# Kernel optimization log

Measured on AMD Instinct MI355X. Metric: run time of the kernel, lower is better.

## Reference

```python
import jax, jax.numpy as jnp
import numpy as np

HIDDEN = 1024
INTER = 4096

def setup_inputs() -> dict:
    key = jax.random.key(0)
    k1, k2, k3, k4, k5 = jax.random.split(key, 5)
    hidden_states = jax.random.normal(k1, (4, 2048, HIDDEN), dtype=jnp.float32)
    # Linear params: W stored pre-transposed as [in, out], matching W = dense.weight.t()
    W1 = jax.random.normal(k2, (HIDDEN, INTER), dtype=jnp.float32) * (1.0 / np.sqrt(HIDDEN))
    b1 = jax.random.normal(k3, (INTER,), dtype=jnp.float32) * 0.02
    W2 = jax.random.normal(k4, (INTER, HIDDEN), dtype=jnp.float32) * (1.0 / np.sqrt(INTER))
    b2 = jax.random.normal(k5, (HIDDEN,), dtype=jnp.float32) * 0.02
    return {"hidden_states": hidden_states, "W1": W1, "b1": b1, "W2": W2, "b2": b2}

def reference(hidden_states, W1, b1, W2, b2):
    # Tiled loops in the original are exactly a dense 2-layer MLP with ReLU.
    h = jax.nn.relu(jnp.einsum('bsh,hi->bsi', hidden_states, W1) + b1)
    return jnp.einsum('bsi,ih->bsh', h, W2) + b2
```

## Files before the change

kernel.cpp:

```cpp
#include <hip/hip_runtime.h>
#include <cstddef>

typedef short short8 __attribute__((ext_vector_type(8)));
typedef unsigned short ushort8 __attribute__((ext_vector_type(8)));
typedef float f32x4 __attribute__((ext_vector_type(4)));

#define AS1(p) ((const __attribute__((address_space(1))) void*)(p))
#define AS3(p) ((__attribute__((address_space(3))) void*)(p))

__device__ __forceinline__ unsigned short f2bf(float f) {
  unsigned int u = __builtin_bit_cast(unsigned int, f);
  u += 0x7FFFu + ((u >> 16) & 1u);
  return (unsigned short)(u >> 16);
}

__device__ __forceinline__ void gload_lds16(const void* g, void* l) {
  __builtin_amdgcn_global_load_lds(AS1(g), AS3(l), 16, 0, 0);
}

__global__ void cvt_f32_bf16(const float* __restrict__ in,
                             unsigned short* __restrict__ out, int n4) {
  int i = blockIdx.x * blockDim.x + threadIdx.x;
  if (i >= n4) return;
  float4 v = *reinterpret_cast<const float4*>(in + (size_t)i * 4);
  ushort4 o;
  o.x = f2bf(v.x); o.y = f2bf(v.y); o.z = f2bf(v.z); o.w = f2bf(v.w);
  *reinterpret_cast<ushort4*>(out + (size_t)i * 4) = o;
}

__global__ void transpose_cvt(const float* __restrict__ in,
                              unsigned short* __restrict__ out,
                              int Kd, int Nd) {
  __shared__ float tile[32][33];
  const int n0 = blockIdx.x * 32;
  const int k0 = blockIdx.y * 32;
  const int tx = threadIdx.x;
  const int ty = threadIdx.y;
#pragma unroll
  for (int i = 0; i < 4; ++i)
    tile[ty + i * 8][tx] = in[(size_t)(k0 + ty + i * 8) * Nd + n0 + tx];
  __syncthreads();
#pragma unroll
  for (int i = 0; i < 4; ++i)
    out[(size_t)(n0 + ty + i * 8) * Kd + k0 + tx] = f2bf(tile[tx][ty + i * 8]);
}

#define PH(ABUF, BBUF, H, KK, STAGE, WAITC)                                    \
  {                                                                            \
    if ((H) == 0) {                                                            \
      _Pragma("unroll")                                                        \
      for (int ni = 0; ni < NB; ++ni)                                          \
        bfr[ni] = *reinterpret_cast<const short8*>((BBUF) + bread[ni][KK]);    \
    }                                                                          \
    short8 afr[4];                                                             \
    _Pragma("unroll")                                                          \
    for (int m2 = 0; m2 < 4; ++m2)                                             \
      afr[m2] = *reinterpret_cast<const short8*>((ABUF) + aread[(H)*4+m2][KK]);\
    STAGE;                                                                     \
    __builtin_amdgcn_s_barrier();                                              \
    asm volatile("s_waitcnt lgkmcnt(0)" ::: "memory");                         \
    __builtin_amdgcn_sched_barrier(0);                                         \
    __builtin_amdgcn_s_setprio(1);                                             \
    _Pragma("unroll")                                                          \
    for (int m2 = 0; m2 < 4; ++m2) {                                           \
      _Pragma("unroll")                                                        \
      for (int ni = 0; ni < NB; ++ni)                                          \
        acc[(H)*4+m2][ni] = __builtin_amdgcn_mfma_f32_16x16x32_bf16(           \
            afr[m2], bfr[ni], acc[(H)*4+m2][ni], 0, 0, 0);                     \
    }                                                                          \
    __builtin_amdgcn_s_setprio(0);                                             \
    WAITC;                                                                     \
    __builtin_amdgcn_s_barrier();                                              \
  }

template <int BN, int RELU_BF16_OUT>
__global__ __launch_bounds__(512, 2)
void gemm8p(const unsigned short* __restrict__ A, int lda,
            const unsigned short* __restrict__ Bp, int ldb,
            const float* __restrict__ bias,
            void* __restrict__ C, int ldc, int K, int nbx) {
  constexpr int PWN     = BN / 4;
  constexpr int NB      = PWN / 16;
  constexpr int LOADS_B = BN / 128;
  constexpr int BHROWS  = BN / 2;
  constexpr int BHSZ    = BHROWS * 128;
  extern __shared__ char lds[];
  char* const A0b = lds;
  char* const A1b = lds + 32768;
  char* const B0b = lds + 65536;
  char* const B1b = lds + 65536 + 2 * BHSZ;

  const int tid  = threadIdx.x;
  const int lane = tid & 63;
  const int wid  = tid >> 6;
  const int wm   = wid >> 2;
  const int wn   = wid & 3;

  const int cpx     = gridDim.x >> 3;
  const int logical = (blockIdx.x & 7) * cpx + (blockIdx.x >> 3);
  const int bx = logical % nbx;
  const int by = logical / nbx;
  const int m0 = by * 256;
  const int n0 = bx * BN;

  f32x4 acc[8][NB];
#pragma unroll
  for (int i = 0; i < 8; ++i)
#pragma unroll
    for (int j = 0; j < NB; ++j)
      acc[i][j] = (f32x4){0.f, 0.f, 0.f, 0.f};

  size_t aofs0, aofs1, bofs0, bofs1 = 0;
  {
    int sr = tid * 16, nat = sr ^ (((sr >> 7) & 7) << 4);
    aofs0 = (size_t)(m0 + (nat >> 7)) * lda + ((nat & 127) >> 1);
    bofs0 = (size_t)(n0 + (nat >> 7)) * ldb + ((nat & 127) >> 1);
    sr = (512 + tid) * 16; nat = sr ^ (((sr >> 7) & 7) << 4);
    aofs1 = (size_t)(m0 + (nat >> 7)) * lda + ((nat & 127) >> 1);
    if (LOADS_B == 2)
      bofs1 = (size_t)(n0 + (nat >> 7)) * ldb + ((nat & 127) >> 1);
  }
  const int dst0 = (tid & 448) * 16;
  const int dst1 = dst0 + 8192;

  auto stA = [&](char* ab, int half, int kel) {
    gload_lds16(A + aofs0 + (size_t)half * 128 * lda + kel, ab + half * 16384 + dst0);
    gload_lds16(A + aofs1 + (size_t)half * 128 * lda + kel, ab + half * 16384 + dst1);
  };
  auto stB = [&](char* bb, int half, int kel) {
    gload_lds16(Bp + bofs0 + (size_t)half * BHROWS * ldb + kel, bb + half * BHSZ + dst0);
    if constexpr (LOADS_B == 2)
      gload_lds16(Bp + bofs1 + (size_t)half * BHROWS * ldb + kel, bb + half * BHSZ + dst1);
  };
  auto waitLB = [&]() {
    if constexpr (LOADS_B == 2) asm volatile("s_waitcnt vmcnt(2)" ::: "memory");
    else                        asm volatile("s_waitcnt vmcnt(1)" ::: "memory");
  };

  int aread[8][2], bread[NB][2];
#pragma unroll
  for (int mi = 0; mi < 8; ++mi)
#pragma unroll
    for (int kk = 0; kk < 2; ++kk) {
      int nat = (wm * 128 + mi * 16 + (lane & 15)) * 128 + kk * 64 + (lane >> 4) * 16;
      aread[mi][kk] = nat ^ (((nat >> 7) & 7) << 4);
    }
#pragma unroll
  for (int ni = 0; ni < NB; ++ni)
#pragma unroll
    for (int kk = 0; kk < 2; ++kk) {
      int nat = (wn * PWN + ni * 16 + (lane & 15)) * 128 + kk * 64 + (lane >> 4) * 16;
      bread[ni][kk] = nat ^ (((nat >> 7) & 7) << 4);
    }

  stB(B0b, 0, 0);
  stB(B0b, 1, 0);
  stA(A0b, 0, 0);
  stA(A0b, 1, 0);
  stB(B1b, 0, 64);
  waitLB();
  __builtin_amdgcn_s_barrier();

  const int niter = K >> 7;
  for (int it = 0; it < niter; ++it) {
    const bool last = (it == niter - 1);
    const int kb = it << 7;
    short8 bfr[NB];
    PH(A0b, B0b, 0, 0, stB(B1b, 1, kb + 64), ((void)0));
    PH(A0b, B0b, 1, 0, stA(A1b, 0, kb + 64), ((void)0));
    PH(A0b, B0b, 0, 1, stA(A1b, 1, kb + 64), ((void)0));
    PH(A0b, B0b, 1, 1, { if (!last) stB(B0b, 0, kb + 128); },
       { if (last) { asm volatile("s_waitcnt vmcnt(0)" ::: "memory"); } else waitLB(); });
    PH(A1b, B1b, 0, 0, { if (!last) stB(B0b, 1, kb + 128); }, ((void)0));
    PH(A1b, B1b, 1, 0, { if (!last) stA(A0b, 0, kb + 128); }, ((void)0));
    PH(A1b, B1b, 0, 1, { if (!last) stA(A0b, 1, kb + 128); }, ((void)0));
    PH(A1b, B1b, 1, 1, { if (!last) stB(B1b, 0, kb + 192); },
       { if (!last) waitLB(); });
  }

  const int row0 = m0 + wm * 128 + (lane >> 4) * 4;
  const int col0 = n0 + wn * PWN + (lane & 15);
#pragma unroll
  for (int ni = 0; ni < NB; ++ni) {
    const int c = col0 + ni * 16;
    const float bv = bias[c];
#pragma unroll
    for (int mi = 0; mi < 8; ++mi) {
#pragma unroll
      for (int r = 0; r < 4; ++r) {
        const size_t idx = (size_t)(row0 + mi * 16 + r) * ldc + c;
        float v = acc[mi][ni][r] + bv;
        if (RELU_BF16_OUT) {
          v = v > 0.f ? v : 0.f;
          ((unsigned short*)C)[idx] = f2bf(v);
        } else {
          ((float*)C)[idx] = v;
        }
      }
    }
  }
}

template <int A_F32, int RELU_BF16_OUT>
__global__ __launch_bounds__(256, 2)
void gemm_bf16(const void* __restrict__ Ap, int lda,
               const unsigned short* __restrict__ B, int ldb,
               const float* __restrict__ bias,
               void* __restrict__ C, int ldc,
               int K, int beta) {
  __shared__ char lds[32768];
  char* const As = lds;
  char* const Bs = lds + 16384;

  const int tid  = threadIdx.x;
  const int lane = tid & 63;
  const int w    = tid >> 6;
  const int wm   = w >> 1;
  const int wn   = w & 1;
  const int m0   = blockIdx.y * 128;
  const int n0   = blockIdx.x * 128;

  f32x4 acc[4][4];
#pragma unroll
  for (int i = 0; i < 4; ++i)
#pragma unroll
    for (int j = 0; j < 4; ++j)
      acc[i][j] = (f32x4){0.f, 0.f, 0.f, 0.f};

  int srow[4], scol[4], sbase[4];
#pragma unroll
  for (int j = 0; j < 4; ++j) {
    const int stored  = (j * 256 + tid) * 16;
    const int natural = stored ^ (((stored >> 7) & 7) << 4);
    srow[j]  = natural >> 7;
    scol[j]  = (natural & 127) >> 1;
    sbase[j] = (j * 256 + (tid & 192)) * 16;
  }

  size_t agofs[4];
  int ast[4];
  if (A_F32) {
#pragma unroll
    for (int p = 0; p < 4; ++p) {
      const int idx = p * 256 + tid;
      const int r   = idx >> 3;
      const int kbe = (idx & 7) * 8;
      agofs[p] = (size_t)(m0 + r) * lda + kbe;
      const int nat = r * 128 + kbe * 2;
      ast[p] = nat ^ (((nat >> 7) & 7) << 4);
    }
  }

  const int nsteps = K >> 6;
  for (int ks = 0; ks < nsteps; ++ks) {
    const int k0 = ks << 6;
    if (A_F32) {
      const float* Af = (const float*)Ap;
#pragma unroll
      for (int p = 0; p < 4; ++p) {
        const float* s = Af + agofs[p] + k0;
        float4 x0 = *reinterpret_cast<const float4*>(s);
        float4 x1 = *reinterpret_cast<const float4*>(s + 4);
        ushort8 v;
        v[0] = f2bf(x0.x); v[1] = f2bf(x0.y); v[2] = f2bf(x0.z); v[3] = f2bf(x0.w);
        v[4] = f2bf(x1.x); v[5] = f2bf(x1.y); v[6] = f2bf(x1.z); v[7] = f2bf(x1.w);
        *reinterpret_cast<ushort8*>(As + ast[p]) = v;
      }
    } else {
      const unsigned short* Ab = (const unsigned short*)Ap;
#pragma unroll
      for (int j = 0; j < 4; ++j)
        gload_lds16(Ab + (size_t)(m0 + srow[j]) * lda + (k0 + scol[j]),
                    As + sbase[j]);
    }
#pragma unroll
    for (int j = 0; j < 4; ++j)
      gload_lds16(B + (size_t)(n0 + srow[j]) * ldb + (k0 + scol[j]),
                  Bs + sbase[j]);
    __syncthreads();

#pragma unroll
    for (int kk = 0; kk < 2; ++kk) {
      const int kb = kk * 64 + (lane >> 4) * 16;
      short8 af[4], bfv[4];
#pragma unroll
      for (int mi = 0; mi < 4; ++mi) {
        int nat = (wm * 64 + mi * 16 + (lane & 15)) * 128 + kb;
        int st  = nat ^ (((nat >> 7) & 7) << 4);
        af[mi] = *reinterpret_cast<const short8*>(As + st);
      }
#pragma unroll
      for (int ni = 0; ni < 4; ++ni) {
        int nat = (wn * 64 + ni * 16 + (lane & 15)) * 128 + kb;
        int st  = nat ^ (((nat >> 7) & 7) << 4);
        bfv[ni] = *reinterpret_cast<const short8*>(Bs + st);
      }
#pragma unroll
      for (int mi = 0; mi < 4; ++mi)
#pragma unroll
        for (int ni = 0; ni < 4; ++ni)
          acc[mi][ni] = __builtin_amdgcn_mfma_f32_16x16x32_bf16(
              af[mi], bfv[ni], acc[mi][ni], 0, 0, 0);
    }
    __syncthreads();
  }

  const int row0 = m0 + wm * 64 + (lane >> 4) * 4;
  const int col0 = n0 + wn * 64 + (lane & 15);
#pragma unroll
  for (int ni = 0; ni < 4; ++ni) {
    const int c = col0 + ni * 16;
    const float bv = beta ? 0.f : bias[c];
#pragma unroll
    for (int mi = 0; mi < 4; ++mi) {
#pragma unroll
      for (int r = 0; r < 4; ++r) {
        const size_t idx = (size_t)(row0 + mi * 16 + r) * ldc + c;
        float v = acc[mi][ni][r] + bv;
        if (RELU_BF16_OUT) {
          v = v > 0.f ? v : 0.f;
          ((unsigned short*)C)[idx] = f2bf(v);
        } else {
          if (beta) v += ((float*)C)[idx];
          ((float*)C)[idx] = v;
        }
      }
    }
  }
}

extern "C" void kernel_launch(void* const* d_in, const int* in_sizes, int n_in,
                              void* d_out, int out_size, void* d_ws, size_t ws_size,
                              hipStream_t stream) {
  const float* X  = (const float*)d_in[0];
  const float* W1 = (const float*)d_in[1];
  const float* b1 = (const float*)d_in[2];
  const float* W2 = (const float*)d_in[3];
  const float* b2 = (const float*)d_in[4];
  float* out = (float*)d_out;

  const int M = 8192, H = 1024, I = 4096;
  const size_t MB = 1024 * 1024;

  char* ws = (char*)d_ws;
  unsigned short* W1t = (unsigned short*)ws;
  unsigned short* W2t = (unsigned short*)(ws + 8 * MB);

  transpose_cvt<<<dim3(I / 32, H / 32), dim3(32, 8), 0, stream>>>(W1, W1t, H, I);
  transpose_cvt<<<dim3(H / 32, I / 32), dim3(32, 8), 0, stream>>>(W2, W2t, I, H);

  if (ws_size >= 80 * MB) {
    unsigned short* Xbf = (unsigned short*)((char*)d_out + 16 * MB);
    unsigned short* Hbf = (unsigned short*)(ws + 16 * MB);
    int n4 = (M * H) / 4;
    cvt_f32_bf16<<<(n4 + 255) / 256, 256, 0, stream>>>(X, Xbf, n4);
    gemm8p<256, 1><<<512, 512, 131072, stream>>>(Xbf, H, W1t, H, b1, Hbf, I, H, I / 256);
    gemm8p<128, 0><<<256, 512, 98304, stream>>>(Hbf, I, W2t, I, b2, out, H, I, H / 128);
    return;
  }

  int Ic, useXbf;
  unsigned short* Xbf = nullptr;
  unsigned short* Hc;
  if (ws_size >= 64 * MB) {
    Ic = 2048; useXbf = 1;
    Xbf = (unsigned short*)(ws + 16 * MB);
    Hc  = (unsigned short*)(ws + 32 * MB);
  } else if (ws_size >= 48 * MB) {
    Ic = 1024; useXbf = 1;
    Xbf = (unsigned short*)(ws + 16 * MB);
    Hc  = (unsigned short*)(ws + 32 * MB);
  } else if (ws_size >= 32 * MB) {
    Ic = 1024; useXbf = 0;
    Hc  = (unsigned short*)(ws + 16 * MB);
  } else if (ws_size >= 24 * MB) {
    Ic = 512;  useXbf = 0;
    Hc  = (unsigned short*)(ws + 16 * MB);
  } else if (ws_size >= 20 * MB) {
    Ic = 256;  useXbf = 0;
    Hc  = (unsigned short*)(ws + 16 * MB);
  } else {
    Ic = 128;  useXbf = 0;
    Hc  = (unsigned short*)(ws + 16 * MB);
  }

  if (useXbf) {
    int n4 = (M * H) / 4;
    cvt_f32_bf16<<<(n4 + 255) / 256, 256, 0, stream>>>(X, Xbf, n4);
  }

  const int nch = I / Ic;
  for (int c = 0; c < nch; ++c) {
    const int i0 = c * Ic;
    if (useXbf)
      gemm_bf16<0, 1><<<dim3(Ic / 128, M / 128), 256, 0, stream>>>(
          Xbf, H, W1t + (size_t)i0 * H, H, b1 + i0, Hc, Ic, H, 0);
    else
      gemm_bf16<1, 1><<<dim3(Ic / 128, M / 128), 256, 0, stream>>>(
          X, H, W1t + (size_t)i0 * H, H, b1 + i0, Hc, Ic, H, 0);
    gemm_bf16<0, 0><<<dim3(H / 128, M / 128), 256, 0, stream>>>(
        Hc, Ic, W2t + i0, I, b2, out, H, Ic, c > 0);
  }
}
```

Baseline: 165.4 us.

## Restage GEMM LDS buffers by K-half for finer-grained prefetch pipeline

```diff
diff --git a/kernel.cpp b/kernel.cpp
--- a/kernel.cpp
+++ b/kernel.cpp
@@ -16,6 +16,11 @@
 
 __device__ __forceinline__ void gload_lds16(const void* g, void* l) {
   __builtin_amdgcn_global_load_lds(AS1(g), AS3(l), 16, 0, 0);
+}
+
+template <int N>
+__device__ __forceinline__ void vwait() {
+  asm volatile("s_waitcnt vmcnt(%0)" :: "n"(N) : "memory");
 }
 
 __global__ void cvt_f32_bf16(const float* __restrict__ in,
@@ -45,18 +50,21 @@
     out[(size_t)(n0 + ty + i * 8) * Kd + k0 + tx] = f2bf(tile[tx][ty + i * 8]);
 }
 
-#define PH(ABUF, BBUF, H, KK, STAGE, WAITC)                                    \
+#define PHASE(D, KK, MH, STAGE, WAIT)                                          \
   {                                                                            \
-    if ((H) == 0) {                                                            \
+    char* ab = lds + (D) * 32768 + (KK) * 16384;                               \
+    if ((MH) == 0) {                                                           \
+      char* bb = lds + 65536 + (D) * 2 * BKH + (KK) * BKH;                     \
       _Pragma("unroll")                                                        \
       for (int ni = 0; ni < NB; ++ni)                                          \
-        bfr[ni] = *reinterpret_cast<const short8*>((BBUF) + bread[ni][KK]);    \
+        bfr[ni] = *reinterpret_cast<const short8*>(bb + brd[ni]);              \
     }                                                                          \
     short8 afr[4];                                                             \
     _Pragma("unroll")                                                          \
     for (int m2 = 0; m2 < 4; ++m2)                                             \
-      afr[m2] = *reinterpret_cast<const short8*>((ABUF) + aread[(H)*4+m2][KK]);\
+      afr[m2] = *reinterpret_cast<const short8*>(ab + ard[(MH) * 4 + m2]);     \
     STAGE;                                                                     \
+    __builtin_amdgcn_sched_barrier(0);                                         \
     __builtin_amdgcn_s_barrier();                                              \
     asm volatile("s_waitcnt lgkmcnt(0)" ::: "memory");                         \
     __builtin_amdgcn_sched_barrier(0);                                         \
@@ -65,30 +73,27 @@
     for (int m2 = 0; m2 < 4; ++m2) {                                           \
       _Pragma("unroll")                                                        \
       for (int ni = 0; ni < NB; ++ni)                                          \
-        acc[(H)*4+m2][ni] = __builtin_amdgcn_mfma_f32_16x16x32_bf16(           \
-            afr[m2], bfr[ni], acc[(H)*4+m2][ni], 0, 0, 0);                     \
+        acc[(MH) * 4 + m2][ni] = __builtin_amdgcn_mfma_f32_16x16x32_bf16(      \
+            afr[m2], bfr[ni], acc[(MH) * 4 + m2][ni], 0, 0, 0);                \
     }                                                                          \
     __builtin_amdgcn_s_setprio(0);                                             \
-    WAITC;                                                                     \
+    WAIT;                                                                      \
     __builtin_amdgcn_s_barrier();                                              \
   }
 
 template <int BN, int RELU_BF16_OUT>
 __global__ __launch_bounds__(512, 2)
-void gemm8p(const unsigned short* __restrict__ A, int lda,
-            const unsigned short* __restrict__ Bp, int ldb,
-            const float* __restrict__ bias,
-            void* __restrict__ C, int ldc, int K, int nbx) {
+void gemm_kh(const unsigned short* __restrict__ A, int lda,
+             const unsigned short* __restrict__ B, int ldb,
+             const float* __restrict__ bias,
+             void* __restrict__ C, int ldc, int K, int nbx) {
+  constexpr int NB      = BN / 64;
   constexpr int PWN     = BN / 4;
-  constexpr int NB      = PWN / 16;
-  constexpr int LOADS_B = BN / 128;
-  constexpr int BHROWS  = BN / 2;
-  constexpr int BHSZ    = BHROWS * 128;
+  constexpr int BKH     = BN * 64;
+  constexpr int BL      = BN / 128;
+  constexpr int WSTEADY = 2 + 2 * BL;
+  constexpr int NSH     = (BN == 256) ? 7 : 6;
   extern __shared__ char lds[];
-  char* const A0b = lds;
-  char* const A1b = lds + 32768;
-  char* const B0b = lds + 65536;
-  char* const B1b = lds + 65536 + 2 * BHSZ;
 
   const int tid  = threadIdx.x;
   const int lane = tid & 63;
@@ -110,72 +115,83 @@
     for (int j = 0; j < NB; ++j)
       acc[i][j] = (f32x4){0.f, 0.f, 0.f, 0.f};
 
-  size_t aofs0, aofs1, bofs0, bofs1 = 0;
+  size_t aG[2];
+  size_t bG[2];
+#pragma unroll
+  for (int u = 0; u < 2; ++u) {
+    const int s    = (u * 512 + tid) * 16;
+    const int nat  = s ^ (((s >> 7) & 7) << 4);
+    const int line = nat >> 7;
+    const int boff = nat & 127;
+    const int sub  = (boff >> 6) & 1;
+    const int kel  = (boff & 63) >> 1;
+    aG[u] = (size_t)(m0 + sub * 128 + line) * lda + kel;
+    if (u < BL) {
+      const int brow = sub * (BN / 2) + line;
+      bG[u] = (size_t)(n0 + brow) * ldb + kel;
+    } else {
+      bG[u] = 0;
+    }
+  }
+  const int wbase = wid * 1024;
+
+  auto stage_a = [&](int d, int kk, int t) {
+    char* dst = lds + d * 32768 + kk * 16384;
+    const size_t kofs = (size_t)t * 64 + kk * 32;
+    gload_lds16(A + aG[0] + kofs, dst + wbase);
+    gload_lds16(A + aG[1] + kofs, dst + 8192 + wbase);
+  };
+  auto stage_b = [&](int d, int kk, int t) {
+    char* dst = lds + 65536 + d * 2 * BKH + kk * BKH;
+    const size_t kofs = (size_t)t * 64 + kk * 32;
+    gload_lds16(B + bG[0] + kofs, dst + wbase);
+    if constexpr (BL == 2)
+      gload_lds16(B + bG[1] + kofs, dst + 8192 + wbase);
+  };
+
+  int ard[8], brd[NB];
+#pragma unroll
+  for (int mi = 0; mi < 8; ++mi) {
+    const int row  = wm * 128 + mi * 16 + (lane & 15);
+    const int nat  = (row & 127) * 128 + (row >> 7) * 64 + (lane >> 4) * 16;
+    ard[mi] = nat ^ (((nat >> 7) & 7) << 4);
+  }
+#pragma unroll
+  for (int ni = 0; ni < NB; ++ni) {
+    const int row  = wn * PWN + ni * 16 + (lane & 15);
+    const int nat  = (row & ((BN / 2) - 1)) * 128 + (row >> NSH) * 64 +
+                     (lane >> 4) * 16;
+    brd[ni] = nat ^ (((nat >> 7) & 7) << 4);
+  }
+
+  stage_b(0, 0, 0); stage_a(0, 0, 0); stage_b(0, 1, 0); stage_a(0, 1, 0);
+  stage_b(1, 0, 1); stage_a(1, 0, 1); stage_b(1, 1, 1);
+  vwait<WSTEADY>();
+  __builtin_amdgcn_s_barrier();
+
+  const int ni_ = (K >> 7);
+  short8 bfr[NB];
+  for (int it = 0; it < ni_ - 1; ++it) {
+    const int t = it << 1;
+    PHASE(0, 0, 0, stage_a(1, 1, t + 1), );
+    PHASE(0, 0, 1, stage_b(0, 0, t + 2), );
+    PHASE(0, 1, 0, stage_a(0, 0, t + 2), );
+    PHASE(0, 1, 1, stage_b(0, 1, t + 2), vwait<WSTEADY>());
+    PHASE(1, 0, 0, stage_a(0, 1, t + 2), );
+    PHASE(1, 0, 1, stage_b(1, 0, t + 3), );
+    PHASE(1, 1, 0, stage_a(1, 0, t + 3), );
+    PHASE(1, 1, 1, stage_b(1, 1, t + 3), vwait<WSTEADY>());
+  }
   {
-    int sr = tid * 16, nat = sr ^ (((sr >> 7) & 7) << 4);
-    aofs0 = (size_t)(m0 + (nat >> 7)) * lda + ((nat & 127) >> 1);
-    bofs0 = (size_t)(n0 + (nat >> 7)) * ldb + ((nat & 127) >> 1);
-    sr = (512 + tid) * 16; nat = sr ^ (((sr >> 7) & 7) << 4);
-    aofs1 = (size_t)(m0 + (nat >> 7)) * lda + ((nat & 127) >> 1);
-    if (LOADS_B == 2)
-      bofs1 = (size_t)(n0 + (nat >> 7)) * ldb + ((nat & 127) >> 1);
-  }
-  const int dst0 = (tid & 448) * 16;
-  const int dst1 = dst0 + 8192;
-
-  auto stA = [&](char* ab, int half, int kel) {
-    gload_lds16(A + aofs0 + (size_t)half * 128 * lda + kel, ab + half * 16384 + dst0);
-    gload_lds16(A + aofs1 + (size_t)half * 128 * lda + kel, ab + half * 16384 + dst1);
-  };
-  auto stB = [&](char* bb, int half, int kel) {
-    gload_lds16(Bp + bofs0 + (size_t)half * BHROWS * ldb + kel, bb + half * BHSZ + dst0);
-    if constexpr (LOADS_B == 2)
-      gload_lds16(Bp + bofs1 + (size_t)half * BHROWS * ldb + kel, bb + half * BHSZ + dst1);
-  };
-  auto waitLB = [&]() {
-    if constexpr (LOADS_B == 2) asm volatile("s_waitcnt vmcnt(2)" ::: "memory");
-    else                        asm volatile("s_waitcnt vmcnt(1)" ::: "memory");
-  };
-
-  int aread[8][2], bread[NB][2];
-#pragma unroll
-  for (int mi = 0; mi < 8; ++mi)
-#pragma unroll
-    for (int kk = 0; kk < 2; ++kk) {
-      int nat = (wm * 128 + mi * 16 + (lane & 15)) * 128 + kk * 64 + (lane >> 4) * 16;
-      aread[mi][kk] = nat ^ (((nat >> 7) & 7) << 4);
-    }
-#pragma unroll
-  for (int ni = 0; ni < NB; ++ni)
-#pragma unroll
-    for (int kk = 0; kk < 2; ++kk) {
-      int nat = (wn * PWN + ni * 16 + (lane & 15)) * 128 + kk * 64 + (lane >> 4) * 16;
-      bread[ni][kk] = nat ^ (((nat >> 7) & 7) << 4);
-    }
-
-  stB(B0b, 0, 0);
-  stB(B0b, 1, 0);
-  stA(A0b, 0, 0);
-  stA(A0b, 1, 0);
-  stB(B1b, 0, 64);
-  waitLB();
-  __builtin_amdgcn_s_barrier();
-
-  const int niter = K >> 7;
-  for (int it = 0; it < niter; ++it) {
-    const bool last = (it == niter - 1);
-    const int kb = it << 7;
-    short8 bfr[NB];
-    PH(A0b, B0b, 0, 0, stB(B1b, 1, kb + 64), ((void)0));
-    PH(A0b, B0b, 1, 0, stA(A1b, 0, kb + 64), ((void)0));
-    PH(A0b, B0b, 0, 1, stA(A1b, 1, kb + 64), ((void)0));
-    PH(A0b, B0b, 1, 1, { if (!last) stB(B0b, 0, kb + 128); },
-       { if (last) { asm volatile("s_waitcnt vmcnt(0)" ::: "memory"); } else waitLB(); });
-    PH(A1b, B1b, 0, 0, { if (!last) stB(B0b, 1, kb + 128); }, ((void)0));
-    PH(A1b, B1b, 1, 0, { if (!last) stA(A0b, 0, kb + 128); }, ((void)0));
-    PH(A1b, B1b, 0, 1, { if (!last) stA(A0b, 1, kb + 128); }, ((void)0));
-    PH(A1b, B1b, 1, 1, { if (!last) stB(B1b, 0, kb + 192); },
-       { if (!last) waitLB(); });
+    const int tl = (ni_ << 1) - 1;
+    PHASE(0, 0, 0, stage_a(1, 1, tl), );
+    PHASE(0, 0, 1, , );
+    PHASE(0, 1, 0, , );
+    PHASE(0, 1, 1, , vwait<0>());
+    PHASE(1, 0, 0, , );
+    PHASE(1, 0, 1, , );
+    PHASE(1, 1, 0, , );
+    PHASE(1, 1, 1, , );
   }
 
   const int row0 = m0 + wm * 128 + (lane >> 4) * 4;
@@ -241,13 +257,13 @@
   int ast[4];
   if (A_F32) {
 #pragma unroll
-    for (int p = 0; p < 4; ++p) {
-      const int idx = p * 256 + tid;
-      const int r   = idx >> 3;
+    for (int pq = 0; pq < 4; ++pq) {
+      const int idx = pq * 256 + tid;
+      const int rr  = idx >> 3;
       const int kbe = (idx & 7) * 8;
-      agofs[p] = (size_t)(m0 + r) * lda + kbe;
-      const int nat = r * 128 + kbe * 2;
-      ast[p] = nat ^ (((nat >> 7) & 7) << 4);
+      agofs[pq] = (size_t)(m0 + rr) * lda + kbe;
+      const int nat = rr * 128 + kbe * 2;
+      ast[pq] = nat ^ (((nat >> 7) & 7) << 4);
     }
   }
 
@@ -257,14 +273,14 @@
     if (A_F32) {
       const float* Af = (const float*)Ap;
 #pragma unroll
-      for (int p = 0; p < 4; ++p) {
-        const float* s = Af + agofs[p] + k0;
-        float4 x0 = *reinterpret_cast<const float4*>(s);
-        float4 x1 = *reinterpret_cast<const float4*>(s + 4);
+      for (int pq = 0; pq < 4; ++pq) {
+        const float* sp = Af + agofs[pq] + k0;
+        float4 x0 = *reinterpret_cast<const float4*>(sp);
+        float4 x1 = *reinterpret_cast<const float4*>(sp + 4);
         ushort8 v;
         v[0] = f2bf(x0.x); v[1] = f2bf(x0.y); v[2] = f2bf(x0.z); v[3] = f2bf(x0.w);
         v[4] = f2bf(x1.x); v[5] = f2bf(x1.y); v[6] = f2bf(x1.z); v[7] = f2bf(x1.w);
-        *reinterpret_cast<ushort8*>(As + ast[p]) = v;
+        *reinterpret_cast<ushort8*>(As + ast[pq]) = v;
       }
     } else {
       const unsigned short* Ab = (const unsigned short*)Ap;
@@ -314,9 +330,9 @@
 #pragma unroll
     for (int mi = 0; mi < 4; ++mi) {
 #pragma unroll
-      for (int r = 0; r < 4; ++r) {
-        const size_t idx = (size_t)(row0 + mi * 16 + r) * ldc + c;
-        float v = acc[mi][ni][r] + bv;
+      for (int rr = 0; rr < 4; ++rr) {
+        const size_t idx = (size_t)(row0 + mi * 16 + rr) * ldc + c;
+        float v = acc[mi][ni][rr] + bv;
         if (RELU_BF16_OUT) {
           v = v > 0.f ? v : 0.f;
           ((unsigned short*)C)[idx] = f2bf(v);
@@ -354,8 +370,10 @@
     unsigned short* Hbf = (unsigned short*)(ws + 16 * MB);
     int n4 = (M * H) / 4;
     cvt_f32_bf16<<<(n4 + 255) / 256, 256, 0, stream>>>(X, Xbf, n4);
-    gemm8p<256, 1><<<512, 512, 131072, stream>>>(Xbf, H, W1t, H, b1, Hbf, I, H, I / 256);
-    gemm8p<128, 0><<<256, 512, 98304, stream>>>(Hbf, I, W2t, I, b2, out, H, I, H / 128);
+    gemm_kh<256, 1><<<512, 512, 131072, stream>>>(
+        Xbf, H, W1t, H, b1, Hbf, I, H, I / 256);
+    gemm_kh<128, 0><<<256, 512, 98304, stream>>>(
+        Hbf, I, W2t, I, b2, out, H, I, H / 128);
     return;
   }
 
```

Result: slower. 169.0 us (+2.1%).
